# Optimization experiments

Measured on AMD Instinct MI355X. Metric: run time of the kernel, lower is better.

## Reference

```python
import jax, jax.numpy as jnp
import numpy as np
from jax import lax

B, N, T, NX = 4, 512, 24, 8
H = 64
PRED_LEN, NY = 12, 1
E_RAND = 8192
EPS = 1e-5


def setup_inputs() -> dict:
    key = jax.random.key(0)
    ks = jax.random.split(key, 24)
    sc = lambda k, shape: (jax.random.normal(k, shape, jnp.float32) * 0.05)
    x = jax.random.normal(ks[0], (B, N, T, NX), jnp.float32)
    er = jax.random.randint(ks[1], (2, E_RAND), 0, N, dtype=jnp.int32)
    loops = jnp.stack([jnp.arange(N, dtype=jnp.int32), jnp.arange(N, dtype=jnp.int32)])
    edge_index = jnp.concatenate([er, loops], axis=1)  # [2, 8704]
    return {
        'x': x,
        'edge_index': edge_index,
        'W_fc': sc(ks[2], (NX, H)), 'b_fc': jnp.zeros((H,), jnp.float32),
        'W1': sc(ks[3], (H, H)), 'a_l1': sc(ks[4], (H,)), 'a_r1': sc(ks[5], (H,)), 'bias1': jnp.zeros((H,), jnp.float32),
        'W2': sc(ks[6], (H, H)), 'a_l2': sc(ks[7], (H,)), 'a_r2': sc(ks[8], (H,)), 'bias2': jnp.zeros((H,), jnp.float32),
        'W_ih': sc(ks[9], (4 * H, H)), 'W_hh': sc(ks[10], (4 * H, H)),
        'b_ih': jnp.zeros((4 * H,), jnp.float32), 'b_hh': jnp.zeros((4 * H,), jnp.float32),
        'g_l': jnp.ones((H,), jnp.float32), 'b_l': jnp.zeros((H,), jnp.float32),
        'g_g': jnp.ones((H,), jnp.float32), 'b_g': jnp.zeros((H,), jnp.float32),
        'W_d': sc(ks[11], (H, PRED_LEN * NY)), 'b_d': jnp.zeros((PRED_LEN * NY,), jnp.float32),
    }


def _layer_norm(x, g, b):
    mu = jnp.mean(x, axis=-1, keepdims=True)
    var = jnp.mean(jnp.square(x - mu), axis=-1, keepdims=True)
    return (x - mu) * lax.rsqrt(var + EPS) * g + b


def _gat(x, W, a_l, a_r, bias, mask):
    # x: [B,N,T,F] -> operate in [B,T,N,H] layout (torch transpose(1,2))
    h = jnp.einsum('bntf,fh->btnh', x, W)          # [B,T,N,H]
    el = jnp.einsum('btnh,h->btn', h, a_l)          # attn_l
    er = jnp.einsum('btnh,h->btn', h, a_r)          # attn_r
    e = el[..., :, None] + er[..., None, :]         # [B,T,N,N]
    e = jax.nn.leaky_relu(e, negative_slope=0.2)
    e = jnp.where(mask, e, -jnp.inf)
    alpha = jax.nn.softmax(e, axis=-1)
    out = jnp.einsum('btmn,btnh->bmth', alpha, h) + bias  # back to [B,N,T,H]
    return jax.nn.gelu(out, approximate=False)


def _lstm(xseq, W_ih, W_hh, b_ih, b_hh):
    # xseq: [M, T, H] -> outputs [M, T, H]; PyTorch gate order i,f,g,o
    M = xseq.shape[0]
    Hh = W_hh.shape[1]
    b = b_ih + b_hh
    def step(carry, xt):
        hprev, cprev = carry
        gates = xt @ W_ih.T + hprev @ W_hh.T + b
        i, f, g, o = jnp.split(gates, 4, axis=-1)
        c = jax.nn.sigmoid(f) * cprev + jax.nn.sigmoid(i) * jnp.tanh(g)
        h = jax.nn.sigmoid(o) * jnp.tanh(c)
        return (h, c), h
    init = (jnp.zeros((M, Hh), xseq.dtype), jnp.zeros((M, Hh), xseq.dtype))
    _, hs = lax.scan(step, init, xseq.transpose(1, 0, 2))  # [T,M,H]
    return hs.transpose(1, 0, 2)


def reference(x, edge_index, W_fc, b_fc, W1, a_l1, a_r1, bias1, W2, a_l2, a_r2, bias2,
              W_ih, W_hh, b_ih, b_hh, g_l, b_l, g_g, b_g, W_d, b_d):
    Bb, Nn, Tt, _ = x.shape
    mask = jnp.zeros((Nn, Nn), bool).at[edge_index[0], edge_index[1]].set(True)
    x_h = jnp.einsum('bntf,fh->bnth', x, W_fc) + b_fc          # fc
    g1 = _gat(x_h, W1, a_l1, a_r1, bias1, mask)                # conv1
    g2 = _gat(g1, W2, a_l2, a_r2, bias2, mask)                 # conv2
    l = _lstm(x_h.reshape(Bb * Nn, Tt, -1), W_ih, W_hh, b_ih, b_hh).reshape(Bb, Nn, Tt, -1)
    h = _layer_norm(g2, g_g, b_g) + _layer_norm(l, g_l, b_l)
    last = h[:, :, -1, :]                                       # [B,N,H]
    out = last @ W_d + b_d                                      # [B,N,pred_len*ny]
    return out.reshape(Bb, Nn, PRED_LEN, NY)
```

## Files before the change

kernel.cpp:

```cpp
#include <hip/hip_runtime.h>
#include <hip/hip_bf16.h>
#include <math.h>

#define BB 4
#define NN 512
#define TT 24
#define NXF 8
#define HH 64
#define PRED 12
#define MM (BB*NN)

typedef __attribute__((ext_vector_type(8))) short short8;
typedef __attribute__((ext_vector_type(4))) float f32x4;
typedef unsigned short ushort;

#define WS_H1THI  0
#define WS_H1TLO  65536
#define WS_H2THI  131072
#define WS_H2TLO  196608
#define WS_HL     262144
#define WS_EL     393216
#define WS_ER     395264
#define WS_EL2    397312
#define WS_ER2    399360
#define WS_WCOMB  401408
#define WS_BCOMB  403456
#define WS_WHHFRAG 403712
#define WS_MASK   411904

__device__ inline float sigm(float x){ return 1.f/(1.f+__expf(-x)); }
__device__ inline float tanh_fast(float x){ float e=__expf(2.f*x); return 1.f - 2.f/(e+1.f); }
__device__ inline float gelu_exact(float x){ return 0.5f*x*(1.f+erff(x*0.70710678118654752440f)); }
__device__ inline ushort f2bu(float f){
    unsigned b=__float_as_uint(f);
    return (ushort)((b + 0x7FFFu + ((b>>16)&1u))>>16);
}
__device__ inline float bu2f(ushort u){ return __uint_as_float(((unsigned)u)<<16); }

__global__ __launch_bounds__(256,2) void gat1pre_kernel(
    const float* __restrict__ x, const float* __restrict__ Wfc, const float* __restrict__ bfc,
    const float* __restrict__ W1, const float* __restrict__ al1, const float* __restrict__ ar1,
    const float* __restrict__ Wih, const float* __restrict__ Whh,
    const float* __restrict__ bih, const float* __restrict__ bhh,
    const int* __restrict__ ei, int E,
    ushort* __restrict__ H1Thi, ushort* __restrict__ H1Tlo,
    float* __restrict__ el, float* __restrict__ er,
    float* __restrict__ wcombG, float* __restrict__ bcombG,
    ushort* __restrict__ whhfrag, unsigned* __restrict__ maskG)
{
    __shared__ float sw1[HH*HH];
    __shared__ float swfc[NXF*HH];
    __shared__ float sb[HH], sal[HH], sar[HH];
    __shared__ float sxh[4][68];
    __shared__ float sx[4][NXF];
    __shared__ unsigned msk[NN*16/2];
    const int t = threadIdx.x;

    if (blockIdx.x >= 520){
        for (int i = t; i < 8192; i += 256) msk[i] = 0u;
        __syncthreads();
        for (int e = t; e < E; e += 256){
            int s = ei[e];
            int d = ei[E + e];
            atomicOr(&msk[s*16 + (d>>5)], 1u << (d & 31));
        }
        __syncthreads();
        for (int i = t; i < 8192; i += 256) maskG[i] = msk[i];
        return;
    }

    if (blockIdx.x >= 512){
        const int f = blockIdx.x - 512;
        const int ng = t;
        float accf = 0.f, accb = 0.f;
        const float* wr = Wih + ng*64;
        #pragma unroll
        for (int k = 0; k < 64; ++k){
            float wv = wr[k];
            accf += Wfc[f*64 + k] * wv;
            accb += bfc[k] * wv;
        }
        wcombG[f*256 + ng] = accf;
        if (f == 0) bcombG[ng] = accb + bih[ng] + bhh[ng];
        #pragma unroll
        for (int u = 0; u < 8; ++u){
            int o = f*2048 + u*256 + t;
            int F  = o >> 9;
            int ln = (o >> 3) & 63;
            int j  = o & 7;
            int w_ = F >> 3, tt = (F >> 1) & 3, ks = F & 1;
            int q = ln >> 4, c = ln & 15;
            int ngx = (w_ + 4*tt)*16 + c;
            whhfrag[o] = f2bu(Whh[ngx*64 + ks*32 + q*8 + j]);
        }
        return;
    }

    const int r = t >> 6, h = t & 63;
    #pragma unroll
    for (int i = 0; i < 16; ++i) sw1[t + 256*i] = W1[t + 256*i];
    swfc[t] = Wfc[t];
    swfc[t+256] = Wfc[t+256];
    if (t < 64) sb[t] = bfc[t];
    else if (t < 128) sal[t-64] = al1[t-64];
    else if (t < 192) sar[t-128] = ar1[t-128];
    if (t < 32){
        int rr = t >> 3, f = t & 7;
        sx[rr][f] = x[(size_t)(blockIdx.x*4 + rr)*(TT*NXF) + (TT-1)*NXF + f];
    }
    __syncthreads();
    float xh = sb[h];
    #pragma unroll
    for (int f = 0; f < NXF; ++f) xh += sx[r][f]*swfc[f*HH + h];
    sxh[r][h] = xh;
    __syncthreads();
    float acc = 0.f;
    const float4* xr = (const float4*)&sxh[r][0];
    #pragma unroll
    for (int k4 = 0; k4 < 16; ++k4){
        float4 xv = xr[k4];
        acc += xv.x*sw1[(4*k4+0)*HH+h] + xv.y*sw1[(4*k4+1)*HH+h]
             + xv.z*sw1[(4*k4+2)*HH+h] + xv.w*sw1[(4*k4+3)*HH+h];
    }
    const int m = blockIdx.x*4 + r;
    {
        ushort hh = f2bu(acc);
        size_t o = ((size_t)(m >> 9)*HH + h)*NN + (m & (NN-1));
        H1Thi[o] = hh;
        H1Tlo[o] = f2bu(acc - bu2f(hh));
    }
    float v1 = acc*sal[h], v2 = acc*sar[h];
    #pragma unroll
    for (int o = 32; o; o >>= 1){ v1 += __shfl_xor(v1,o); v2 += __shfl_xor(v2,o); }
    if (h == 0){ el[m] = v1; er[m] = v2; }
}

#define LHS 72
#define LXS 40
__global__ __launch_bounds__(256,2) void mid_fused_kernel(
    const ushort* __restrict__ H1Thi, const ushort* __restrict__ H1Tlo,
    const float* __restrict__ el_in, const float* __restrict__ er_in,
    const unsigned* __restrict__ maskG,
    const float* __restrict__ bias1,
    const float* __restrict__ W2, const float* __restrict__ al2, const float* __restrict__ ar2,
    ushort* __restrict__ H2Thi, ushort* __restrict__ H2Tlo,
    float* __restrict__ el2, float* __restrict__ er2,
    const float* __restrict__ x,
    const float* __restrict__ wcombG, const float* __restrict__ bcombG,
    const ushort* __restrict__ whhfrag,
    float* __restrict__ hl)
{
    __shared__ __align__(16) char smem[41216];
    const int t = threadIdx.x;
    const int lane = t & 63;
    const int w = t >> 6;
    const int quad = lane >> 4;
    const int c16 = lane & 15;

    if (blockIdx.x >= 128){
        ushort* hbi = (ushort*)smem;
        ushort* hlo = (ushort*)(smem + 4608);
        ushort* xls = (ushort*)(smem + 9216);
        const int m0 = (blockIdx.x - 128) * 16;

        {
            unsigned* h0 = (unsigned*)hbi;
            unsigned* l0 = (unsigned*)hlo;
            for (int i = t; i < 2*16*LHS/2; i += 256){ h0[i] = 0u; l0[i] = 0u; }
            unsigned* xw = (unsigned*)xls;
            for (int i = t; i < TT*16*LXS/2; i += 256) xw[i] = 0u;
        }
        short8 bw[4][2]; short8 bx[4]; float bc[4];
        #pragma unroll
        for (int tt = 0; tt < 4; ++tt){
            const int ng = (w + 4*tt)*16 + c16;
            bc[tt] = bcombG[ng];
            #pragma unroll
            for (int ks = 0; ks < 2; ++ks)
                bw[tt][ks] = *(const short8*)&whhfrag[(((w*4+tt)*2)+ks)*512 + lane*8];
            short8 vx = {0,0,0,0,0,0,0,0};
            if (quad == 0){
                #pragma unroll
                for (int j = 0; j < 8; ++j) vx[j] = (short)f2bu(wcombG[j*256 + ng]);
            }
            bx[tt] = vx;
        }
        __syncthreads();
        for (int i = t; i < 16*TT*NXF; i += 256){
            int r = i / (TT*NXF);
            int rem = i - r*(TT*NXF);
            int st = rem >> 3, f = rem & 7;
            xls[st*(16*LXS) + r*LXS + f] = f2bu(x[(size_t)(m0+r)*(TT*NXF) + rem]);
        }
        __syncthreads();

        float cst[4] = {0,0,0,0};
        float hf[4]  = {0,0,0,0};

        for (int st = 0; st < TT; ++st){
            const int p = st & 1;
            const ushort* hb  = hbi + p*(16*LHS);
            const ushort* hl_ = hlo + p*(16*LHS);
            short8 ahi0 = *(const short8*)&hb[c16*LHS + quad*8];
            short8 ahi1 = *(const short8*)&hb[c16*LHS + 32 + quad*8];
            short8 alo0 = *(const short8*)&hl_[c16*LHS + quad*8];
            short8 alo1 = *(const short8*)&hl_[c16*LHS + 32 + quad*8];
            short8 ax   = *(const short8*)&xls[st*(16*LXS) + c16*LXS + quad*8];
            f32x4 acc[4];
            #pragma unroll
            for (int tt = 0; tt < 4; ++tt){
                f32x4 a = {bc[tt], bc[tt], bc[tt], bc[tt]};
                a = __builtin_amdgcn_mfma_f32_16x16x32_bf16(ax,   bx[tt],    a, 0,0,0);
                a = __builtin_amdgcn_mfma_f32_16x16x32_bf16(ahi0, bw[tt][0], a, 0,0,0);
                a = __builtin_amdgcn_mfma_f32_16x16x32_bf16(ahi1, bw[tt][1], a, 0,0,0);
                a = __builtin_amdgcn_mfma_f32_16x16x32_bf16(alo0, bw[tt][0], a, 0,0,0);
                a = __builtin_amdgcn_mfma_f32_16x16x32_bf16(alo1, bw[tt][1], a, 0,0,0);
                acc[tt] = a;
            }
            ushort* ho   = hbi + (p^1)*(16*LHS);
            ushort* lo_o = hlo + (p^1)*(16*LHS);
            #pragma unroll
            for (int reg = 0; reg < 4; ++reg){
                float gi = acc[0][reg], gf = acc[1][reg], gg = acc[2][reg], go = acc[3][reg];
                float cn = sigm(gf)*cst[reg] + sigm(gi)*tanh_fast(gg);
                cst[reg] = cn;
                float hn = sigm(go)*tanh_fast(cn);
                hf[reg] = hn;
                ushort hu = f2bu(hn);
                float lov = hn - bu2f(hu);
                int addr = (quad*4+reg)*LHS + w*16 + c16;
                ho[addr] = hu;
                lo_o[addr] = f2bu(lov);
            }
            __syncthreads();
        }
        #pragma unroll
        for (int reg = 0; reg < 4; ++reg)
            hl[(size_t)(m0 + quad*4 + reg)*HH + w*16 + c16] = hf[reg];
        return;
    }

    unsigned (*smask)[16] = (unsigned(*)[16])smem;
    float* er_s  = (float*)(smem + 1024);
    float* sal   = (float*)(smem + 3072);
    float* sar   = (float*)(smem + 3328);
    ushort (*ahi)[520] = (ushort(*)[520])(smem + 3584);
    ushort (*alo_)[520] = (ushort(*)[520])(smem + 20224);
    float (*xh2)[68] = (float(*)[68])(smem + 36864);
    float* sw2 = (float*)(smem + 3584);

    const int b = blockIdx.x >> 5;
    const int m0 = (blockIdx.x & 31) * 16;
    const int l = lane;

    if (t < 64) sal[t] = al2[t]; else if (t < 128) sar[t-64] = ar2[t-64];
    ((unsigned*)smask)[t] = maskG[m0*16 + t];
    er_s[t] = er_in[b*NN + t];
    er_s[t+256] = er_in[b*NN + t + 256];
    __syncthreads();
    for (int q = 0; q < 4; ++q){
        const int i = w*4 + q;
        const float elv = el_in[b*NN + m0 + i];
        float e8[8]; unsigned mk = 0; float mx = -1e30f;
        #pragma unroll
        for (int j = 0; j < 8; ++j){
            int n = l + 64*j;
            float ev = elv + er_s[n];
            ev = ev >= 0.f ? ev : 0.2f*ev;
            unsigned mb = (smask[i][(l>>5) + 2*j] >> (l & 31)) & 1u;
            e8[j] = ev;
            if (mb){ mk |= (1u<<j); mx = fmaxf(mx, ev); }
        }
        #pragma unroll
        for (int o = 32; o; o >>= 1) mx = fmaxf(mx, __shfl_xor(mx, o));
        float s = 0.f;
        #pragma unroll
        for (int j = 0; j < 8; ++j){
            float p = ((mk>>j) & 1u) ? __expf(e8[j]-mx) : 0.f;
            e8[j] = p; s += p;
        }
        #pragma unroll
        for (int o = 32; o; o >>= 1) s += __shfl_xor(s, o);
        const float inv = 1.f/s;
        #pragma unroll
        for (int j = 0; j < 8; ++j){
            float p = e8[j]*inv;
            ushort ph = f2bu(p);
            ahi[i][l + 64*j] = ph;
            alo_[i][l + 64*j] = f2bu(p - bu2f(ph));
        }
    }
    __syncthreads();

    f32x4 acc = {0.f,0.f,0.f,0.f};
    {
        const ushort* bhiP = H1Thi + ((size_t)b*HH + w*16 + c16)*NN + quad*8;
        const ushort* bloP = H1Tlo + ((size_t)b*HH + w*16 + c16)*NN + quad*8;
        const ushort* ahiP = &ahi[c16][quad*8];
        const ushort* aloP = &alo_[c16][quad*8];
        #pragma unroll
        for (int kk = 0; kk < 16; ++kk){
            short8 fa_hi = *(const short8*)(ahiP + kk*32);
            short8 fa_lo = *(const short8*)(aloP + kk*32);
            short8 fb_hi = *(const short8*)(bhiP + kk*32);
            short8 fb_lo = *(const short8*)(bloP + kk*32);
            acc = __builtin_amdgcn_mfma_f32_16x16x32_bf16(fa_hi, fb_hi, acc, 0,0,0);
            acc = __builtin_amdgcn_mfma_f32_16x16x32_bf16(fa_lo, fb_hi, acc, 0,0,0);
            acc = __builtin_amdgcn_mfma_f32_16x16x32_bf16(fa_hi, fb_lo, acc, 0,0,0);
        }
    }
    {
        const int h = w*16 + c16;
        const float bv = bias1[h];
        #pragma unroll
        for (int reg = 0; reg < 4; ++reg)
            xh2[quad*4 + reg][h] = gelu_exact(acc[reg] + bv);
    }
    __syncthreads();
    #pragma unroll
    for (int i = 0; i < 16; ++i) sw2[t + 256*i] = W2[t + 256*i];
    __syncthreads();
    {
        const int h = l;
        for (int q = 0; q < 4; ++q){
            const int i = w + 4*q;
            float acc2 = 0.f;
            const float4* xr = (const float4*)&xh2[i][0];
            #pragma unroll
            for (int k4 = 0; k4 < 16; ++k4){
                float4 xv = xr[k4];
                acc2 += xv.x*sw2[(4*k4+0)*HH+h] + xv.y*sw2[(4*k4+1)*HH+h]
                      + xv.z*sw2[(4*k4+2)*HH+h] + xv.w*sw2[(4*k4+3)*HH+h];
            }
            const int m = m0 + i;
            {
                ushort vh = f2bu(acc2);
                size_t o = ((size_t)b*HH + h)*NN + m;
                H2Thi[o] = vh;
                H2Tlo[o] = f2bu(acc2 - bu2f(vh));
            }
            float v1 = acc2*sal[h], v2 = acc2*sar[h];
            #pragma unroll
            for (int o = 32; o; o >>= 1){ v1 += __shfl_xor(v1,o); v2 += __shfl_xor(v2,o); }
            if (h == 0){ el2[b*NN + m] = v1; er2[b*NN + m] = v2; }
        }
    }
}

__global__ __launch_bounds__(256,2) void attn2_final_kernel(
    const ushort* __restrict__ H2Thi, const ushort* __restrict__ H2Tlo,
    const float* __restrict__ el_in, const float* __restrict__ er_in,
    const unsigned* __restrict__ maskG,
    const float* __restrict__ bias2,
    const float* __restrict__ hl,
    const float* __restrict__ g_l, const float* __restrict__ b_l,
    const float* __restrict__ g_g, const float* __restrict__ b_g,
    const float* __restrict__ W_d, const float* __restrict__ b_d,
    float* __restrict__ out)
{
    __shared__ __align__(16) char smem[40448];
    unsigned (*smask)[16] = (unsigned(*)[16])smem;
    float* er_s  = (float*)(smem + 1024);
    ushort (*ahi)[520] = (ushort(*)[520])(smem + 3072);
    ushort (*alo_)[520] = (ushort(*)[520])(smem + 19712);
    float* sg2  = (float*)(smem + 36352);
    float* sdec = (float*)(smem + 3072);

    const int t = threadIdx.x;
    const int b = blockIdx.x >> 5;
    const int m0 = (blockIdx.x & 31) * 16;
    const int l = t & 63, w = t >> 6;
    const int quad = l >> 4, c16 = l & 15;

    ((unsigned*)smask)[t] = maskG[m0*16 + t];
    er_s[t] = er_in[b*NN + t];
    er_s[t+256] = er_in[b*NN + t + 256];
    __syncthreads();
    for (int q = 0; q < 4; ++q){
        const int i = w*4 + q;
        const float elv = el_in[b*NN + m0 + i];
        float e8[8]; unsigned mk = 0; float mx = -1e30f;
        #pragma unroll
        for (int j = 0; j < 8; ++j){
            int n = l + 64*j;
            float ev = elv + er_s[n];
            ev = ev >= 0.f ? ev : 0.2f*ev;
            unsigned mb = (smask[i][(l>>5) + 2*j] >> (l & 31)) & 1u;
            e8[j] = ev;
            if (mb){ mk |= (1u<<j); mx = fmaxf(mx, ev); }
        }
        #pragma unroll
        for (int o = 32; o; o >>= 1) mx = fmaxf(mx, __shfl_xor(mx, o));
        float s = 0.f;
        #pragma unroll
        for (int j = 0; j < 8; ++j){
            float p = ((mk>>j) & 1u) ? __expf(e8[j]-mx) : 0.f;
            e8[j] = p; s += p;
        }
        #pragma unroll
        for (int o = 32; o; o >>= 1) s += __shfl_xor(s, o);
        const float inv = 1.f/s;
        #pragma unroll
        for (int j = 0; j < 8; ++j){
            float p = e8[j]*inv;
            ushort ph = f2bu(p);
            ahi[i][l + 64*j] = ph;
            alo_[i][l + 64*j] = f2bu(p - bu2f(ph));
        }
    }
    __syncthreads();

    f32x4 acc = {0.f,0.f,0.f,0.f};
    {
        const ushort* bhiP = H2Thi + ((size_t)b*HH + w*16 + c16)*NN + quad*8;
        const ushort* bloP = H2Tlo + ((size_t)b*HH + w*16 + c16)*NN + quad*8;
        const ushort* ahiP = &ahi[c16][quad*8];
        const ushort* aloP = &alo_[c16][quad*8];
        #pragma unroll
        for (int kk = 0; kk < 16; ++kk){
            short8 fa_hi = *(const short8*)(ahiP + kk*32);
            short8 fa_lo = *(const short8*)(aloP + kk*32);
            short8 fb_hi = *(const short8*)(bhiP + kk*32);
            short8 fb_lo = *(const short8*)(bloP + kk*32);
            acc = __builtin_amdgcn_mfma_f32_16x16x32_bf16(fa_hi, fb_hi, acc, 0,0,0);
            acc = __builtin_amdgcn_mfma_f32_16x16x32_bf16(fa_lo, fb_hi, acc, 0,0,0);
            acc = __builtin_amdgcn_mfma_f32_16x16x32_bf16(fa_hi, fb_lo, acc, 0,0,0);
        }
    }
    {
        const int h = w*16 + c16;
        const float bv = bias2[h];
        #pragma unroll
        for (int reg = 0; reg < 4; ++reg)
            sg2[(quad*4 + reg)*HH + h] = gelu_exact(acc[reg] + bv);
    }
    __syncthreads();
    const int gbase = b*NN + m0;
    {
        const int h = l;
        for (int q = 0; q < 4; ++q){
            const int ml = w*4 + q;
            float gv = sg2[ml*HH + h];
            float lv = hl[(size_t)(gbase + ml)*HH + h];

            float s1 = gv;
            #pragma unroll
            for (int o = 32; o; o >>= 1) s1 += __shfl_xor(s1, o);
            float dg = gv - s1*(1.f/64.f);
            float v1 = dg*dg;
            #pragma unroll
            for (int o = 32; o; o >>= 1) v1 += __shfl_xor(v1, o);
            float lng = dg*rsqrtf(v1*(1.f/64.f) + 1e-5f)*g_g[h] + b_g[h];

            float s2 = lv;
            #pragma unroll
            for (int o = 32; o; o >>= 1) s2 += __shfl_xor(s2, o);
            float dl = lv - s2*(1.f/64.f);
            float v2 = dl*dl;
            #pragma unroll
            for (int o = 32; o; o >>= 1) v2 += __shfl_xor(v2, o);
            float lnl = dl*rsqrtf(v2*(1.f/64.f) + 1e-5f)*g_l[h] + b_l[h];

            sdec[ml*HH + h] = lng + lnl;
        }
    }
    __syncthreads();
    if (t < 16*PRED){
        int rr = t / PRED, pp = t - rr*PRED;
        float a = b_d[pp];
        #pragma unroll
        for (int k = 0; k < HH; ++k) a += sdec[rr*HH + k]*W_d[k*PRED + pp];
        out[(size_t)(gbase + rr)*PRED + pp] = a;
    }
}

extern "C" void kernel_launch(void* const* d_in, const int* in_sizes, int n_in,
                              void* d_out, int out_size, void* d_ws, size_t ws_size,
                              hipStream_t stream){
    const float* x    = (const float*)d_in[0];
    const int*   ei   = (const int*)  d_in[1];
    const float* Wfc  = (const float*)d_in[2];
    const float* bfc  = (const float*)d_in[3];
    const float* W1   = (const float*)d_in[4];
    const float* al1  = (const float*)d_in[5];
    const float* ar1  = (const float*)d_in[6];
    const float* bias1= (const float*)d_in[7];
    const float* W2   = (const float*)d_in[8];
    const float* al2  = (const float*)d_in[9];
    const float* ar2  = (const float*)d_in[10];
    const float* bias2= (const float*)d_in[11];
    const float* Wih  = (const float*)d_in[12];
    const float* Whh  = (const float*)d_in[13];
    const float* bih  = (const float*)d_in[14];
    const float* bhh  = (const float*)d_in[15];
    const float* g_l  = (const float*)d_in[16];
    const float* b_l  = (const float*)d_in[17];
    const float* g_g  = (const float*)d_in[18];
    const float* b_g  = (const float*)d_in[19];
    const float* W_d  = (const float*)d_in[20];
    const float* b_d  = (const float*)d_in[21];

    float* ws = (float*)d_ws;
    const int E = in_sizes[1] / 2;

    gat1pre_kernel<<<521, 256, 0, stream>>>(x, Wfc, bfc, W1, al1, ar1,
                                            Wih, Whh, bih, bhh,
                                            ei, E,
                                            (ushort*)(ws+WS_H1THI), (ushort*)(ws+WS_H1TLO),
                                            ws+WS_EL, ws+WS_ER,
                                            ws+WS_WCOMB, ws+WS_BCOMB,
                                            (ushort*)(ws+WS_WHHFRAG),
                                            (unsigned*)(ws+WS_MASK));
    mid_fused_kernel<<<256, 256, 0, stream>>>((const ushort*)(ws+WS_H1THI), (const ushort*)(ws+WS_H1TLO),
                                              ws+WS_EL, ws+WS_ER,
                                              (const unsigned*)(ws+WS_MASK),
                                              bias1, W2, al2, ar2,
                                              (ushort*)(ws+WS_H2THI), (ushort*)(ws+WS_H2TLO),
                                              ws+WS_EL2, ws+WS_ER2,
                                              x, ws+WS_WCOMB, ws+WS_BCOMB,
                                              (const ushort*)(ws+WS_WHHFRAG),
                                              ws+WS_HL);
    attn2_final_kernel<<<BB*(NN/16), 256, 0, stream>>>((const ushort*)(ws+WS_H2THI), (const ushort*)(ws+WS_H2TLO),
                                                       ws+WS_EL2, ws+WS_ER2,
                                                       (const unsigned*)(ws+WS_MASK),
                                                       bias2, ws+WS_HL,
                                                       g_l, b_l, g_g, b_g, W_d, b_d,
                                                       (float*)d_out);
}
```

Measured before the change: 152.7 us.

## Stage transposed H1/H2 bf16 outputs in shared memory for coalesced stores

```diff
diff --git a/kernel.cpp b/kernel.cpp
--- a/kernel.cpp
+++ b/kernel.cpp
@@ -8,7 +8,6 @@
 #define NXF 8
 #define HH 64
 #define PRED 12
-#define MM (BB*NN)
 
 typedef __attribute__((ext_vector_type(8))) short short8;
 typedef __attribute__((ext_vector_type(4))) float f32x4;
@@ -44,19 +43,16 @@
     const float* __restrict__ bih, const float* __restrict__ bhh,
     const int* __restrict__ ei, int E,
     ushort* __restrict__ H1Thi, ushort* __restrict__ H1Tlo,
-    float* __restrict__ el, float* __restrict__ er,
+    float* __restrict__ elG, float* __restrict__ erG,
     float* __restrict__ wcombG, float* __restrict__ bcombG,
     ushort* __restrict__ whhfrag, unsigned* __restrict__ maskG)
 {
-    __shared__ float sw1[HH*HH];
-    __shared__ float swfc[NXF*HH];
-    __shared__ float sb[HH], sal[HH], sar[HH];
-    __shared__ float sxh[4][68];
-    __shared__ float sx[4][NXF];
-    __shared__ unsigned msk[NN*16/2];
+    __shared__ __align__(16) char smem[32768];
     const int t = threadIdx.x;
-
-    if (blockIdx.x >= 520){
+    const int blk = blockIdx.x;
+
+    if (blk == 136){
+        unsigned* msk = (unsigned*)smem;
         for (int i = t; i < 8192; i += 256) msk[i] = 0u;
         __syncthreads();
         for (int e = t; e < E; e += 256){
@@ -69,8 +65,8 @@
         return;
     }
 
-    if (blockIdx.x >= 512){
-        const int f = blockIdx.x - 512;
+    if (blk >= 128){
+        const int f = blk - 128;
         const int ng = t;
         float accf = 0.f, accb = 0.f;
         const float* wr = Wih + ng*64;
@@ -96,7 +92,22 @@
         return;
     }
 
-    const int r = t >> 6, h = t & 63;
+    const int lane = t & 63;
+    const int w = t >> 6;
+    const int b   = blk >> 5;
+    const int m0l = (blk & 31) * 16;
+    const int m0g = blk * 16;
+
+    float* sw1  = (float*)smem;
+    float* swfc = (float*)(smem + 16384);
+    float* sb   = (float*)(smem + 18432);
+    float* sal  = (float*)(smem + 18688);
+    float* sar  = (float*)(smem + 18944);
+    float (*sx)[NXF] = (float(*)[NXF])(smem + 19200);
+    float (*sxh)[68] = (float(*)[68])(smem + 19712);
+    ushort (*thi)[68] = (ushort(*)[68])(smem + 24064);
+    ushort (*tlo)[68] = (ushort(*)[68])(smem + 26240);
+
     #pragma unroll
     for (int i = 0; i < 16; ++i) sw1[t + 256*i] = W1[t + 256*i];
     swfc[t] = Wfc[t];
@@ -104,35 +115,47 @@
     if (t < 64) sb[t] = bfc[t];
     else if (t < 128) sal[t-64] = al1[t-64];
     else if (t < 192) sar[t-128] = ar1[t-128];
-    if (t < 32){
+    if (t < 128){
         int rr = t >> 3, f = t & 7;
-        sx[rr][f] = x[(size_t)(blockIdx.x*4 + rr)*(TT*NXF) + (TT-1)*NXF + f];
-    }
-    __syncthreads();
-    float xh = sb[h];
+        sx[rr][f] = x[(size_t)(m0g + rr)*(TT*NXF) + (TT-1)*NXF + f];
+    }
+    __syncthreads();
     #pragma unroll
-    for (int f = 0; f < NXF; ++f) xh += sx[r][f]*swfc[f*HH + h];
-    sxh[r][h] = xh;
-    __syncthreads();
-    float acc = 0.f;
-    const float4* xr = (const float4*)&sxh[r][0];
+    for (int rr = 0; rr < 4; ++rr){
+        const int row = w*4 + rr;
+        float v = sb[lane];
+        #pragma unroll
+        for (int f = 0; f < NXF; ++f) v += sx[row][f]*swfc[f*HH + lane];
+        sxh[row][lane] = v;
+    }
+    __syncthreads();
     #pragma unroll
-    for (int k4 = 0; k4 < 16; ++k4){
-        float4 xv = xr[k4];
-        acc += xv.x*sw1[(4*k4+0)*HH+h] + xv.y*sw1[(4*k4+1)*HH+h]
-             + xv.z*sw1[(4*k4+2)*HH+h] + xv.w*sw1[(4*k4+3)*HH+h];
-    }
-    const int m = blockIdx.x*4 + r;
-    {
+    for (int rr = 0; rr < 4; ++rr){
+        const int row = w*4 + rr;
+        float acc = 0.f;
+        const float4* xr = (const float4*)&sxh[row][0];
+        #pragma unroll
+        for (int k4 = 0; k4 < 16; ++k4){
+            float4 xv = xr[k4];
+            acc += xv.x*sw1[(4*k4+0)*HH+lane] + xv.y*sw1[(4*k4+1)*HH+lane]
+                 + xv.z*sw1[(4*k4+2)*HH+lane] + xv.w*sw1[(4*k4+3)*HH+lane];
+        }
         ushort hh = f2bu(acc);
-        size_t o = ((size_t)(m >> 9)*HH + h)*NN + (m & (NN-1));
-        H1Thi[o] = hh;
-        H1Tlo[o] = f2bu(acc - bu2f(hh));
-    }
-    float v1 = acc*sal[h], v2 = acc*sar[h];
+        thi[row][lane] = hh;
+        tlo[row][lane] = f2bu(acc - bu2f(hh));
+        float v1 = acc*sal[lane], v2 = acc*sar[lane];
+        #pragma unroll
+        for (int o = 32; o; o >>= 1){ v1 += __shfl_xor(v1,o); v2 += __shfl_xor(v2,o); }
+        if (lane == 0){ elG[m0g + row] = v1; erG[m0g + row] = v2; }
+    }
+    __syncthreads();
     #pragma unroll
-    for (int o = 32; o; o >>= 1){ v1 += __shfl_xor(v1,o); v2 += __shfl_xor(v2,o); }
-    if (h == 0){ el[m] = v1; er[m] = v2; }
+    for (int p = 0; p < 4; ++p){
+        int hh2 = (t >> 4) + 16*p, n2 = t & 15;
+        size_t og = ((size_t)b*HH + hh2)*NN + m0l + n2;
+        H1Thi[og] = thi[n2][hh2];
+        H1Tlo[og] = tlo[n2][hh2];
+    }
 }
 
 #define LHS 72
@@ -150,7 +173,7 @@
     const ushort* __restrict__ whhfrag,
     float* __restrict__ hl)
 {
-    __shared__ __align__(16) char smem[41216];
+    __shared__ __align__(16) char smem[45568];
     const int t = threadIdx.x;
     const int lane = t & 63;
     const int w = t >> 6;
@@ -247,6 +270,8 @@
     ushort (*ahi)[520] = (ushort(*)[520])(smem + 3584);
     ushort (*alo_)[520] = (ushort(*)[520])(smem + 20224);
     float (*xh2)[68] = (float(*)[68])(smem + 36864);
+    ushort (*th2)[68] = (ushort(*)[68])(smem + 41216);
+    ushort (*tl2)[68] = (ushort(*)[68])(smem + 43392);
     float* sw2 = (float*)(smem + 3584);
 
     const int b = blockIdx.x >> 5;
@@ -332,18 +357,22 @@
                 acc2 += xv.x*sw2[(4*k4+0)*HH+h] + xv.y*sw2[(4*k4+1)*HH+h]
                       + xv.z*sw2[(4*k4+2)*HH+h] + xv.w*sw2[(4*k4+3)*HH+h];
             }
-            const int m = m0 + i;
-            {
-                ushort vh = f2bu(acc2);
-                size_t o = ((size_t)b*HH + h)*NN + m;
-                H2Thi[o] = vh;
-                H2Tlo[o] = f2bu(acc2 - bu2f(vh));
-            }
+            ushort vh = f2bu(acc2);
+            th2[i][h] = vh;
+            tl2[i][h] = f2bu(acc2 - bu2f(vh));
             float v1 = acc2*sal[h], v2 = acc2*sar[h];
             #pragma unroll
             for (int o = 32; o; o >>= 1){ v1 += __shfl_xor(v1,o); v2 += __shfl_xor(v2,o); }
-            if (h == 0){ el2[b*NN + m] = v1; er2[b*NN + m] = v2; }
-        }
+            if (h == 0){ el2[b*NN + m0 + i] = v1; er2[b*NN + m0 + i] = v2; }
+        }
+    }
+    __syncthreads();
+    #pragma unroll
+    for (int p = 0; p < 4; ++p){
+        int hh2 = (t >> 4) + 16*p, n2 = t & 15;
+        size_t og = ((size_t)b*HH + hh2)*NN + m0 + n2;
+        H2Thi[og] = th2[n2][hh2];
+        H2Tlo[og] = tl2[n2][hh2];
     }
 }
 
@@ -503,9 +532,8 @@
     float* ws = (float*)d_ws;
     const int E = in_sizes[1] / 2;
 
-    gat1pre_kernel<<<521, 256, 0, stream>>>(x, Wfc, bfc, W1, al1, ar1,
-                                            Wih, Whh, bih, bhh,
-                                            ei, E,
+    gat1pre_kernel<<<137, 256, 0, stream>>>(x, Wfc, bfc, W1, al1, ar1,
+                                            Wih, Whh, bih, bhh, ei, E,
                                             (ushort*)(ws+WS_H1THI), (ushort*)(ws+WS_H1TLO),
                                             ws+WS_EL, ws+WS_ER,
                                             ws+WS_WCOMB, ws+WS_BCOMB,
```

Result: no change. 151.7 us (-0.6%).
